# Kernel optimization log

Measured on AMD Instinct MI355X. Metric: run time of the kernel, lower is better.

## Reference

```python
import jax, jax.numpy as jnp
import numpy as np
import math

B, S, D, H = 4, 4096, 1024, 128

def setup_inputs() -> dict:
    key = jax.random.key(0)
    ks = jax.random.split(key, 4)
    scale = 1.0 / math.sqrt(D)
    return {
        "inputs": jax.random.normal(ks[0], (B, S, D), dtype=jnp.float32),
        "Wk": jax.random.normal(ks[1], (H, D), dtype=jnp.float32) * scale,
        "bk": jnp.zeros((H,), dtype=jnp.float32),
        "Wq": jax.random.normal(ks[2], (H, D), dtype=jnp.float32) * scale,
        "bq": jnp.zeros((H,), dtype=jnp.float32),
        "Wv": jax.random.normal(ks[3], (H, D), dtype=jnp.float32) * scale,
        "bv": jnp.zeros((H,), dtype=jnp.float32),
        "padding_mask": jnp.ones((B, S), dtype=jnp.int32),
    }

def reference(inputs, Wk, bk, Wq, bq, Wv, bv, padding_mask):
    # Linear projections: [B,S,D] x [H,D]^T -> [B,S,H]
    k = jnp.einsum('bsd,hd->bsh', inputs, Wk) + bk
    q = jnp.einsum('bsd,hd->bsh', inputs, Wq) + bq
    v = jnp.einsum('bsd,hd->bsh', inputs, Wv) + bv
    # Scaled dot-product scores: [B,S,S]
    scores = jnp.einsum('bqh,bkh->bqk', q, k) / jnp.sqrt(jnp.float32(k.shape[-1]))
    # Mask out padded key positions (mask==0 -> -1e9), broadcast over query dim
    scores = jnp.where(padding_mask[:, None, :] == 0, jnp.float32(-1e9), scores)
    weights = jax.nn.softmax(scores, axis=-1)
    # Dropout is identity in eval mode (reference runs inference / training=False)
    out = jnp.einsum('bqk,bkh->bqh', weights, v)
    return out
```

## Files before the change

kernel.cpp:

```cpp
#include <hip/hip_runtime.h>
#include <cmath>

#define B_ 4
#define S_ 4096
#define D_ 1024
#define H_ 128
#define M_ (B_*S_)
#define NQT 32

typedef _Float16 half8 __attribute__((ext_vector_type(8)));
typedef _Float16 half4 __attribute__((ext_vector_type(4)));
typedef float f32x4 __attribute__((ext_vector_type(4)));
typedef int i32x4 __attribute__((ext_vector_type(4)));

#define LOG2E 1.44269504088896340f

__device__ __forceinline__ void gload16(const void* g, void* l) {
    __builtin_amdgcn_global_load_lds(
        (const __attribute__((address_space(1))) unsigned int*)g,
        (__attribute__((address_space(3))) unsigned int*)l,
        16, 0, 0);
}

__global__ __launch_bounds__(256) void conv_w(
    const float* __restrict__ Wq, const float* __restrict__ Wk,
    const float* __restrict__ Wv, _Float16* __restrict__ wh)
{
    const int idx  = blockIdx.x * 256 + threadIdx.x;
    const int base = idx * 8;
    const int m    = base >> 17;
    const int off  = base & ((H_ * D_) - 1);
    const float* src = (m == 0 ? Wq : m == 1 ? Wk : Wv) + off;
    const float4 a = ((const float4*)src)[0];
    const float4 c = ((const float4*)src)[1];
    half8 h = { (_Float16)a.x, (_Float16)a.y, (_Float16)a.z, (_Float16)a.w,
                (_Float16)c.x, (_Float16)c.y, (_Float16)c.z, (_Float16)c.w };
    *(half8*)(wh + base) = h;
}

__global__ __launch_bounds__(256, 3) void proj_kernel(
    const float* __restrict__ x, const _Float16* __restrict__ wh,
    const float* __restrict__ bq, const float* __restrict__ bk,
    const float* __restrict__ bv,
    _Float16* __restrict__ qh, _Float16* __restrict__ kh,
    _Float16* __restrict__ vt)
{
    __shared__ _Float16 Xs[2][64][72];
    __shared__ _Float16 Ws2[2][128][64];

    const int t = threadIdx.x;
    const int yb = blockIdx.y;
    const float* __restrict__ bias = (yb == 0) ? bq : (yb == 1) ? bk : bv;
    const int m0 = blockIdx.x * 64;
    const int w = t >> 6, lane = t & 63;
    const int lg = lane >> 4, lr = lane & 15;

    f32x4 acc[8];
    #pragma unroll
    for (int i = 0; i < 8; ++i) acc[i] = f32x4{0.f, 0.f, 0.f, 0.f};

    const int xrow = t >> 2, xc = (t & 3) * 16;
    const float* xbase = x + (size_t)(m0 + xrow) * D_ + xc;

    int wbyte[4];
    #pragma unroll
    for (int i = 0; i < 4; ++i) {
        const int wrow = 32 * w + 8 * i + (lane >> 3);
        const int wblk = (lane & 7) ^ (lane >> 3);
        wbyte[i] = (wrow * D_ + wblk * 8) * 2;
    }
    const char* whb = (const char*)(wh + (size_t)yb * H_ * D_);

    float4 xfA[4], xfB[4];

#define WISSUE(KT, BUF)                                                       \
    {                                                                         \
        const char* wsrc = whb + (KT) * (64 * 2);                             \
        _Pragma("unroll")                                                     \
        for (int i = 0; i < 4; ++i)                                           \
            gload16(wsrc + wbyte[i], &Ws2[BUF][32 * w + 8 * i][0]);           \
    }
#define XISSUE(KT, XS)                                                        \
    {                                                                         \
        const float4* xs_ = (const float4*)(xbase + (KT) * 64);               \
        _Pragma("unroll") for (int i = 0; i < 4; ++i) XS[i] = xs_[i];         \
    }
#define XWRITE(XS, BUF)                                                       \
    {                                                                         \
        _Pragma("unroll") for (int i = 0; i < 4; ++i) {                       \
            half4 h = { (_Float16)XS[i].x, (_Float16)XS[i].y,                 \
                        (_Float16)XS[i].z, (_Float16)XS[i].w };               \
            *(half4*)&Xs[BUF][xrow][xc + 4 * i] = h;                          \
        }                                                                     \
    }
#define PMFMA(BUF)                                                            \
    {                                                                         \
        _Pragma("unroll") for (int kk = 0; kk < 2; ++kk) {                    \
            half8 a = *(const half8*)&Xs[BUF][w * 16 + lr][kk * 32 + 8 * lg]; \
            _Pragma("unroll") for (int ni = 0; ni < 8; ++ni) {                \
                half8 bfr = *(const half8*)&Ws2[BUF][ni * 16 + lr]            \
                                [((4 * kk + lg) ^ (lr & 7)) * 8];             \
                acc[ni] = __builtin_amdgcn_mfma_f32_16x16x32_f16(a, bfr, acc[ni], 0, 0, 0); \
            }                                                                 \
        }                                                                     \
    }

    WISSUE(0, 0)
    XISSUE(0, xfA)
    XISSUE(1, xfB)
    XWRITE(xfA, 0)
    __syncthreads();

    for (int kt = 0; kt < 16; kt += 2) {
        WISSUE(kt + 1, 1)
        if (kt + 2 < 16) XISSUE(kt + 2, xfA)
        PMFMA(0)
        XWRITE(xfB, 1)
        __syncthreads();
        if (kt + 2 < 16) WISSUE(kt + 2, 0)
        if (kt + 3 < 16) XISSUE(kt + 3, xfB)
        PMFMA(1)
        if (kt + 2 < 16) XWRITE(xfA, 0)
        __syncthreads();
    }
#undef WISSUE
#undef XISSUE
#undef XWRITE
#undef PMFMA

    const float qscale = 0.08838834764831845f * LOG2E;
    const int rowb = m0 + w * 16 + lg * 4;
    #pragma unroll
    for (int ni = 0; ni < 8; ++ni) {
        const int col = ni * 16 + lr;
        const float bval = bias[col];
        if (yb == 0) {
            #pragma unroll
            for (int r = 0; r < 4; ++r)
                qh[(size_t)(rowb + r) * H_ + col] = (_Float16)((acc[ni][r] + bval) * qscale);
        } else if (yb == 1) {
            #pragma unroll
            for (int r = 0; r < 4; ++r)
                kh[(size_t)(rowb + r) * H_ + col] = (_Float16)(acc[ni][r] + bval);
        } else {
            const int bb = rowb >> 12, s0 = rowb & (S_ - 1);
            half4 h;
            #pragma unroll
            for (int r = 0; r < 4; ++r) h[r] = (_Float16)(acc[ni][r] + bval);
            *(half4*)&vt[(size_t)bb * H_ * S_ + (size_t)col * S_ + s0] = h;
        }
    }
}

__device__ __forceinline__ void attn_tile2(
    const _Float16 (&Kb)[64][128], const _Float16 (&Vb)[128][64],
    const half8 (&qf)[2][4], f32x4 (&acc)[2][8], float (&m_)[2], float (&l_)[2],
    int muse, int lg, int lr, bool hi, int idx0, int idx1)
{
    const unsigned long long bz = __ballot(muse == 0);
    f32x4 sf[2][4];
    #pragma unroll
    for (int qs = 0; qs < 2; ++qs)
        #pragma unroll
        for (int i = 0; i < 4; ++i) sf[qs][i] = f32x4{0.f, 0.f, 0.f, 0.f};
    #pragma unroll
    for (int kk = 0; kk < 4; ++kk) {
        #pragma unroll
        for (int ni = 0; ni < 4; ++ni) {
            half8 kb = *(const half8*)&Kb[ni * 16 + lr][((4 * kk + lg) ^ (lr & 7)) * 8];
            #pragma unroll
            for (int qs = 0; qs < 2; ++qs)
                sf[qs][ni] = __builtin_amdgcn_mfma_f32_16x16x32_f16(kb, qf[qs][kk], sf[qs][ni], 0, 0, 0);
        }
    }

    i32x4 pbi[2][2];
    #pragma unroll
    for (int qs = 0; qs < 2; ++qs) {
        if (bz) {
            #pragma unroll
            for (int ni = 0; ni < 4; ++ni) {
                #pragma unroll
                for (int r = 0; r < 4; ++r)
                    if ((bz >> (16 * ni + 4 * lg + r)) & 1ull) sf[qs][ni][r] = -3e9f;
            }
        }
        float tmax = fmaxf(
            fmaxf(fmaxf(fmaxf(sf[qs][0][0], sf[qs][0][1]), fmaxf(sf[qs][0][2], sf[qs][0][3])),
                  fmaxf(fmaxf(sf[qs][1][0], sf[qs][1][1]), fmaxf(sf[qs][1][2], sf[qs][1][3]))),
            fmaxf(fmaxf(fmaxf(sf[qs][2][0], sf[qs][2][1]), fmaxf(sf[qs][2][2], sf[qs][2][3])),
                  fmaxf(fmaxf(sf[qs][3][0], sf[qs][3][1]), fmaxf(sf[qs][3][2], sf[qs][3][3]))));
        tmax = fmaxf(tmax, __shfl_xor(tmax, 16));
        tmax = fmaxf(tmax, __shfl_xor(tmax, 32));
        if (!__all(tmax <= m_[qs] + 8.f)) {
            const float mn  = fmaxf(m_[qs], tmax);
            const float scl = exp2f(m_[qs] - mn);
            m_[qs] = mn; l_[qs] *= scl;
            #pragma unroll
            for (int ni = 0; ni < 8; ++ni) acc[qs][ni] *= scl;
        }
        float rsum = 0.f;
        #pragma unroll
        for (int ni = 0; ni < 4; ++ni) {
            #pragma unroll
            for (int r = 0; r < 4; ++r) {
                const float p = exp2f(sf[qs][ni][r] - m_[qs]);
                sf[qs][ni][r] = p;
                rsum += p;
            }
        }
        rsum += __shfl_xor(rsum, 16);
        rsum += __shfl_xor(rsum, 32);
        l_[qs] += rsum;

        int pk[4][2];
        #pragma unroll
        for (int ni = 0; ni < 4; ++ni) {
            #pragma unroll
            for (int rp = 0; rp < 2; ++rp) {
                auto h2 = __builtin_amdgcn_cvt_pkrtz(sf[qs][ni][2 * rp], sf[qs][ni][2 * rp + 1]);
                pk[ni][rp] = __builtin_bit_cast(int, h2);
            }
        }
        #pragma unroll
        for (int kk = 0; kk < 2; ++kk) {
            #pragma unroll
            for (int dd = 0; dd < 4; ++dd) {
                const int sidx = (dd >> 1) ? idx1 : idx0;
                const int a  = __builtin_amdgcn_ds_bpermute(sidx, pk[2 * kk][dd & 1]);
                const int bb = __builtin_amdgcn_ds_bpermute(sidx, pk[2 * kk + 1][dd & 1]);
                pbi[qs][kk][dd] = hi ? bb : a;
            }
        }
    }
    #pragma unroll
    for (int kk = 0; kk < 2; ++kk) {
        #pragma unroll
        for (int ni = 0; ni < 8; ++ni) {
            half8 vb = *(const half8*)&Vb[ni * 16 + lr][((4 * kk + lg) ^ (lr & 7)) * 8];
            #pragma unroll
            for (int qs = 0; qs < 2; ++qs) {
                const half8 pb = __builtin_bit_cast(half8, pbi[qs][kk]);
                acc[qs][ni] = __builtin_amdgcn_mfma_f32_16x16x32_f16(vb, pb, acc[qs][ni], 0, 0, 0);
            }
        }
    }
}

__global__ __launch_bounds__(256, 2) void attn_kernel(
    const _Float16* __restrict__ qh, const _Float16* __restrict__ kh,
    const _Float16* __restrict__ vt, const int* __restrict__ mask,
    float* __restrict__ pout, float* __restrict__ pm, float* __restrict__ pl,
    const int nsplit)
{
    __shared__ _Float16 Ks[2][64][128];
    __shared__ _Float16 Vs[2][128][64];

    const int t = threadIdx.x;
    const int id = blockIdx.x;
    int qt, sp, b;
    const int ncombo = B_ * nsplit;
    if ((ncombo & 7) == 0) {
        const int per_xcd = ncombo >> 3;
        const int j = id >> 3;
        qt = j & (NQT - 1);
        const int combo = (id & 7) * per_xcd + (j >> 5);
        sp = combo % nsplit; b = combo / nsplit;
    } else {
        qt = id & (NQT - 1);
        const int rest = id >> 5;
        sp = rest % nsplit; b = rest / nsplit;
    }
    const int q0 = qt * 128;
    const int w = t >> 6, lane = t & 63;
    const int lg = lane >> 4, lr = lane & 15;
    const int kvlen  = S_ / nsplit;
    const int iters  = kvlen >> 6;
    const int kvbase = sp * kvlen;

    int kbyte[4], vbyte[4];
    #pragma unroll
    for (int i = 0; i < 4; ++i) {
        const int krow = 16 * w + 4 * i + (lane >> 4);
        const int kblk = (lane & 15) ^ (krow & 7);
        kbyte[i] = (krow * H_ + kblk * 8) * 2;
        const int vrow = 32 * w + 8 * i + (lane >> 3);
        const int vblk = (lane & 7) ^ (lane >> 3);
        vbyte[i] = (vrow * S_ + vblk * 8) * 2;
    }
    const char* kbase_b = (const char*)(kh + (size_t)(b * S_ + kvbase) * H_);
    const char* vbase_b = (const char*)(vt + (size_t)b * H_ * S_ + kvbase);
    const char* mbase_b = (const char*)(mask + b * S_ + kvbase + lane);

#define ISSUE_TILE(IT, NB)                                                    \
    {                                                                         \
        const char* kb_t = kbase_b + (size_t)(IT) * (64 * H_ * 2);            \
        const char* vb_t = vbase_b + (size_t)(IT) * (64 * 2);                 \
        _Pragma("unroll")                                                     \
        for (int i = 0; i < 4; ++i)                                           \
            gload16(kb_t + kbyte[i], &Ks[NB][16 * w + 4 * i][0]);             \
        _Pragma("unroll")                                                     \
        for (int i = 0; i < 4; ++i)                                           \
            gload16(vb_t + vbyte[i], &Vs[NB][32 * w + 8 * i][0]);             \
    }

    half8 qf[2][4];
    #pragma unroll
    for (int qs = 0; qs < 2; ++qs) {
        const _Float16* qp = qh + (size_t)(b * S_ + q0 + w * 32 + qs * 16 + lr) * H_ + 8 * lg;
        #pragma unroll
        for (int kk = 0; kk < 4; ++kk) qf[qs][kk] = *(const half8*)(qp + kk * 32);
    }

    float m_[2] = { -1e30f, -1e30f }, l_[2] = { 0.f, 0.f };
    f32x4 acc[2][8];
    #pragma unroll
    for (int qs = 0; qs < 2; ++qs)
        #pragma unroll
        for (int i = 0; i < 8; ++i) acc[qs][i] = f32x4{0.f, 0.f, 0.f, 0.f};

    const bool hi = (lg >= 2);
    const int idx0 = (16 * ((2 * lg + 0) & 3) + lr) * 4;
    const int idx1 = (16 * ((2 * lg + 1) & 3) + lr) * 4;

    ISSUE_TILE(0, 0)
    int mA = *(const int*)mbase_b;
    int mB = 0;
    __syncthreads();

    for (int it = 0; it < iters; it += 2) {
        if (it + 1 < iters) {
            ISSUE_TILE(it + 1, 1)
            mB = *(const int*)(mbase_b + (size_t)(it + 1) * 256);
        }
        attn_tile2(Ks[0], Vs[0], qf, acc, m_, l_, mA, lg, lr, hi, idx0, idx1);
        __syncthreads();
        if (it + 2 < iters) {
            ISSUE_TILE(it + 2, 0)
            mA = *(const int*)(mbase_b + (size_t)(it + 2) * 256);
        }
        if (it + 1 < iters)
            attn_tile2(Ks[1], Vs[1], qf, acc, m_, l_, mB, lg, lr, hi, idx0, idx1);
        __syncthreads();
    }
#undef ISSUE_TILE

    #pragma unroll
    for (int qs = 0; qs < 2; ++qs) {
        const int qrow = b * S_ + q0 + w * 32 + qs * 16 + lr;
        float* op = pout + (size_t)(sp * M_ + qrow) * H_ + 4 * lg;
        #pragma unroll
        for (int ni = 0; ni < 8; ++ni)
            *(f32x4*)(op + 16 * ni) = acc[qs][ni];
        if (lg == 0) {
            pm[sp * M_ + qrow] = m_[qs];
            pl[sp * M_ + qrow] = l_[qs];
        }
    }
}

__global__ __launch_bounds__(256) void combine_kernel(
    const float* __restrict__ pout, const float* __restrict__ pm,
    const float* __restrict__ pl, float* __restrict__ out, const int nsplit)
{
    const int idx = blockIdx.x * 256 + threadIdx.x;
    const int row = idx >> 7;
    const int h   = idx & (H_ - 1);
    float M = -1e30f;
    for (int sp = 0; sp < nsplit; ++sp) M = fmaxf(M, pm[sp * M_ + row]);
    float Z = 0.f, o = 0.f;
    for (int sp = 0; sp < nsplit; ++sp) {
        const float wgt = exp2f(pm[sp * M_ + row] - M);
        Z += wgt * pl[sp * M_ + row];
        o += wgt * pout[(size_t)(sp * M_ + row) * H_ + h];
    }
    out[idx] = o / Z;
}

extern "C" void kernel_launch(void* const* d_in, const int* in_sizes, int n_in,
                              void* d_out, int out_size, void* d_ws, size_t ws_size,
                              hipStream_t stream)
{
    (void)in_sizes; (void)n_in; (void)out_size;
    const float* x  = (const float*)d_in[0];
    const float* Wk = (const float*)d_in[1];
    const float* bk = (const float*)d_in[2];
    const float* Wq = (const float*)d_in[3];
    const float* bq = (const float*)d_in[4];
    const float* Wv = (const float*)d_in[5];
    const float* bv = (const float*)d_in[6];
    const int* mask = (const int*)d_in[7];

    char* ws = (char*)d_ws;
    const size_t qkvBytes = (size_t)M_ * H_ * sizeof(_Float16);
    _Float16* qh = (_Float16*)ws;
    _Float16* kh = (_Float16*)(ws + qkvBytes);
    _Float16* vt = (_Float16*)(ws + 2 * qkvBytes);
    _Float16* wh = (_Float16*)(ws + 3 * qkvBytes);
    const size_t whBytes = (size_t)3 * H_ * D_ * sizeof(_Float16);
    char* rest = ws + 3 * qkvBytes + whBytes;

    int nsplit = 4;
    const size_t perSplit = (size_t)M_ * H_ * 4 + 2 * (size_t)M_ * 4;
    while (nsplit > 1 &&
           3 * qkvBytes + whBytes + (size_t)nsplit * perSplit > ws_size) nsplit >>= 1;

    float* pout = (float*)rest;
    float* pm   = (float*)(rest + (size_t)nsplit * M_ * H_ * 4);
    float* pl   = pm + (size_t)nsplit * M_;

    conv_w<<<dim3(3 * H_ * D_ / (256 * 8)), 256, 0, stream>>>(Wq, Wk, Wv, wh);
    proj_kernel<<<dim3(M_ / 64, 3), 256, 0, stream>>>(x, wh, bq, bk, bv, qh, kh, vt);
    attn_kernel<<<dim3(NQT * B_ * nsplit), 256, 0, stream>>>(qh, kh, vt, mask, pout, pm, pl, nsplit);
    combine_kernel<<<dim3(M_ * H_ / 256), 256, 0, stream>>>(pout, pm, pl, (float*)d_out, nsplit);
}
```

Measured before the change: 112.5 us.

## Switch attention inner loop to 32x32x16 MFMA with shuffle-based P relayout

Rewrites the per-tile attention computation to use 32x32x16 f16 MFMA instructions instead of 16x16x32, with each wave handling 32 query rows as a single block. The softmax row reductions need only one cross-lane shuffle, and the P-to-operand relayout uses xor-32 shuffles instead of ds_bpermute. The aim is fewer MFMA issues and less cross-lane traffic per tile. In exchange the 16-wide accumulators raise register pressure, and the output stores become scattered float2 writes.

Result: faster. 109.9 us (-2.3%).

```diff
diff --git a/kernel.cpp b/kernel.cpp
--- a/kernel.cpp
+++ b/kernel.cpp
@@ -11,6 +11,7 @@
 typedef _Float16 half8 __attribute__((ext_vector_type(8)));
 typedef _Float16 half4 __attribute__((ext_vector_type(4)));
 typedef float f32x4 __attribute__((ext_vector_type(4)));
+typedef float f32x16 __attribute__((ext_vector_type(16)));
 typedef int i32x4 __attribute__((ext_vector_type(4)));
 
 #define LOG2E 1.44269504088896340f
@@ -152,97 +153,95 @@
     }
 }
 
-__device__ __forceinline__ void attn_tile2(
+__device__ __forceinline__ void attn_tile32(
     const _Float16 (&Kb)[64][128], const _Float16 (&Vb)[128][64],
-    const half8 (&qf)[2][4], f32x4 (&acc)[2][8], float (&m_)[2], float (&l_)[2],
-    int muse, int lg, int lr, bool hi, int idx0, int idx1)
+    const half8 (&qf)[8], f32x16 (&acc2)[4], float& m_, float& l_,
+    int muse, int lane)
 {
     const unsigned long long bz = __ballot(muse == 0);
-    f32x4 sf[2][4];
-    #pragma unroll
-    for (int qs = 0; qs < 2; ++qs)
-        #pragma unroll
-        for (int i = 0; i < 4; ++i) sf[qs][i] = f32x4{0.f, 0.f, 0.f, 0.f};
-    #pragma unroll
-    for (int kk = 0; kk < 4; ++kk) {
-        #pragma unroll
-        for (int ni = 0; ni < 4; ++ni) {
-            half8 kb = *(const half8*)&Kb[ni * 16 + lr][((4 * kk + lg) ^ (lr & 7)) * 8];
+    const int l31 = lane & 31, l7 = lane & 7, hi = lane >> 5;
+
+    f32x16 sf[2];
+    #pragma unroll
+    for (int nb = 0; nb < 2; ++nb)
+        #pragma unroll
+        for (int r = 0; r < 16; ++r) sf[nb][r] = 0.f;
+    #pragma unroll
+    for (int kt = 0; kt < 8; ++kt) {
+        #pragma unroll
+        for (int nb = 0; nb < 2; ++nb) {
+            half8 kb = *(const half8*)&Kb[nb * 32 + l31][((2 * kt + hi) ^ l7) * 8];
+            sf[nb] = __builtin_amdgcn_mfma_f32_32x32x16_f16(kb, qf[kt], sf[nb], 0, 0, 0);
+        }
+    }
+    if (bz) {
+        #pragma unroll
+        for (int nb = 0; nb < 2; ++nb)
             #pragma unroll
-            for (int qs = 0; qs < 2; ++qs)
-                sf[qs][ni] = __builtin_amdgcn_mfma_f32_16x16x32_f16(kb, qf[qs][kk], sf[qs][ni], 0, 0, 0);
-        }
-    }
-
-    i32x4 pbi[2][2];
-    #pragma unroll
-    for (int qs = 0; qs < 2; ++qs) {
-        if (bz) {
-            #pragma unroll
-            for (int ni = 0; ni < 4; ++ni) {
-                #pragma unroll
-                for (int r = 0; r < 4; ++r)
-                    if ((bz >> (16 * ni + 4 * lg + r)) & 1ull) sf[qs][ni][r] = -3e9f;
+            for (int r = 0; r < 16; ++r) {
+                const int kv = nb * 32 + (r & 3) + 8 * (r >> 2) + 4 * hi;
+                if ((bz >> kv) & 1ull) sf[nb][r] = -3e9f;
             }
-        }
-        float tmax = fmaxf(
-            fmaxf(fmaxf(fmaxf(sf[qs][0][0], sf[qs][0][1]), fmaxf(sf[qs][0][2], sf[qs][0][3])),
-                  fmaxf(fmaxf(sf[qs][1][0], sf[qs][1][1]), fmaxf(sf[qs][1][2], sf[qs][1][3]))),
-            fmaxf(fmaxf(fmaxf(sf[qs][2][0], sf[qs][2][1]), fmaxf(sf[qs][2][2], sf[qs][2][3])),
-                  fmaxf(fmaxf(sf[qs][3][0], sf[qs][3][1]), fmaxf(sf[qs][3][2], sf[qs][3][3]))));
-        tmax = fmaxf(tmax, __shfl_xor(tmax, 16));
-        tmax = fmaxf(tmax, __shfl_xor(tmax, 32));
-        if (!__all(tmax <= m_[qs] + 8.f)) {
-            const float mn  = fmaxf(m_[qs], tmax);
-            const float scl = exp2f(m_[qs] - mn);
-            m_[qs] = mn; l_[qs] *= scl;
-            #pragma unroll
-            for (int ni = 0; ni < 8; ++ni) acc[qs][ni] *= scl;
-        }
-        float rsum = 0.f;
-        #pragma unroll
-        for (int ni = 0; ni < 4; ++ni) {
-            #pragma unroll
-            for (int r = 0; r < 4; ++r) {
-                const float p = exp2f(sf[qs][ni][r] - m_[qs]);
-                sf[qs][ni][r] = p;
-                rsum += p;
-            }
-        }
-        rsum += __shfl_xor(rsum, 16);
-        rsum += __shfl_xor(rsum, 32);
-        l_[qs] += rsum;
-
-        int pk[4][2];
-        #pragma unroll
-        for (int ni = 0; ni < 4; ++ni) {
-            #pragma unroll
-            for (int rp = 0; rp < 2; ++rp) {
-                auto h2 = __builtin_amdgcn_cvt_pkrtz(sf[qs][ni][2 * rp], sf[qs][ni][2 * rp + 1]);
-                pk[ni][rp] = __builtin_bit_cast(int, h2);
-            }
-        }
-        #pragma unroll
-        for (int kk = 0; kk < 2; ++kk) {
-            #pragma unroll
-            for (int dd = 0; dd < 4; ++dd) {
-                const int sidx = (dd >> 1) ? idx1 : idx0;
-                const int a  = __builtin_amdgcn_ds_bpermute(sidx, pk[2 * kk][dd & 1]);
-                const int bb = __builtin_amdgcn_ds_bpermute(sidx, pk[2 * kk + 1][dd & 1]);
-                pbi[qs][kk][dd] = hi ? bb : a;
-            }
-        }
-    }
-    #pragma unroll
-    for (int kk = 0; kk < 2; ++kk) {
-        #pragma unroll
-        for (int ni = 0; ni < 8; ++ni) {
-            half8 vb = *(const half8*)&Vb[ni * 16 + lr][((4 * kk + lg) ^ (lr & 7)) * 8];
-            #pragma unroll
-            for (int qs = 0; qs < 2; ++qs) {
-                const half8 pb = __builtin_bit_cast(half8, pbi[qs][kk]);
-                acc[qs][ni] = __builtin_amdgcn_mfma_f32_16x16x32_f16(vb, pb, acc[qs][ni], 0, 0, 0);
-            }
+    }
+    float tmax = sf[0][0];
+    #pragma unroll
+    for (int nb = 0; nb < 2; ++nb)
+        #pragma unroll
+        for (int r = 0; r < 16; ++r) tmax = fmaxf(tmax, sf[nb][r]);
+    tmax = fmaxf(tmax, __shfl_xor(tmax, 32));
+    if (!__all(tmax <= m_ + 8.f)) {
+        const float mn  = fmaxf(m_, tmax);
+        const float scl = exp2f(m_ - mn);
+        m_ = mn; l_ *= scl;
+        #pragma unroll
+        for (int hb = 0; hb < 4; ++hb) acc2[hb] *= scl;
+    }
+    float rsum = 0.f;
+    #pragma unroll
+    for (int nb = 0; nb < 2; ++nb)
+        #pragma unroll
+        for (int r = 0; r < 16; ++r) {
+            const float p = exp2f(sf[nb][r] - m_);
+            sf[nb][r] = p;
+            rsum += p;
+        }
+    rsum += __shfl_xor(rsum, 32);
+    l_ += rsum;
+
+    int pkw[2][8];
+    #pragma unroll
+    for (int nb = 0; nb < 2; ++nb)
+        #pragma unroll
+        for (int i = 0; i < 8; ++i) {
+            auto h2 = __builtin_amdgcn_cvt_pkrtz(sf[nb][2 * i], sf[nb][2 * i + 1]);
+            pkw[nb][i] = __builtin_bit_cast(int, h2);
+        }
+    #pragma unroll
+    for (int nb = 0; nb < 2; ++nb)
+        #pragma unroll
+        for (int hf = 0; hf < 2; ++hf) {
+            const int i0 = hf * 4;
+            const int sA = hi ? pkw[nb][i0 + 0] : pkw[nb][i0 + 2];
+            const int sB = hi ? pkw[nb][i0 + 1] : pkw[nb][i0 + 3];
+            const int rA = __shfl_xor(sA, 32);
+            const int rB = __shfl_xor(sB, 32);
+            const int n0 = hi ? rA : pkw[nb][i0 + 0];
+            const int n1 = hi ? rB : pkw[nb][i0 + 1];
+            const int n2 = hi ? pkw[nb][i0 + 2] : rA;
+            const int n3 = hi ? pkw[nb][i0 + 3] : rB;
+            pkw[nb][i0 + 0] = n0; pkw[nb][i0 + 1] = n1;
+            pkw[nb][i0 + 2] = n2; pkw[nb][i0 + 3] = n3;
+        }
+    #pragma unroll
+    for (int s = 0; s < 4; ++s) {
+        const int nb = s >> 1, hf = s & 1;
+        const half8 pb = __builtin_bit_cast(half8,
+            i32x4{ pkw[nb][hf * 4 + 0], pkw[nb][hf * 4 + 1],
+                   pkw[nb][hf * 4 + 2], pkw[nb][hf * 4 + 3] });
+        #pragma unroll
+        for (int hb = 0; hb < 4; ++hb) {
+            half8 vb = *(const half8*)&Vb[hb * 32 + l31][((2 * s + hi) ^ l7) * 8];
+            acc2[hb] = __builtin_amdgcn_mfma_f32_32x32x16_f16(vb, pb, acc2[hb], 0, 0, 0);
         }
     }
 }
@@ -273,7 +272,7 @@
     }
     const int q0 = qt * 128;
     const int w = t >> 6, lane = t & 63;
-    const int lg = lane >> 4, lr = lane & 15;
+    const int l31 = lane & 31, hi = lane >> 5;
     const int kvlen  = S_ / nsplit;
     const int iters  = kvlen >> 6;
     const int kvbase = sp * kvlen;
@@ -304,24 +303,19 @@
             gload16(vb_t + vbyte[i], &Vs[NB][32 * w + 8 * i][0]);             \
     }
 
-    half8 qf[2][4];
-    #pragma unroll
-    for (int qs = 0; qs < 2; ++qs) {
-        const _Float16* qp = qh + (size_t)(b * S_ + q0 + w * 32 + qs * 16 + lr) * H_ + 8 * lg;
-        #pragma unroll
-        for (int kk = 0; kk < 4; ++kk) qf[qs][kk] = *(const half8*)(qp + kk * 32);
-    }
-
-    float m_[2] = { -1e30f, -1e30f }, l_[2] = { 0.f, 0.f };
-    f32x4 acc[2][8];
-    #pragma unroll
-    for (int qs = 0; qs < 2; ++qs)
-        #pragma unroll
-        for (int i = 0; i < 8; ++i) acc[qs][i] = f32x4{0.f, 0.f, 0.f, 0.f};
-
-    const bool hi = (lg >= 2);
-    const int idx0 = (16 * ((2 * lg + 0) & 3) + lr) * 4;
-    const int idx1 = (16 * ((2 * lg + 1) & 3) + lr) * 4;
+    half8 qf[8];
+    {
+        const _Float16* qp = qh + (size_t)(b * S_ + q0 + 32 * w + l31) * H_ + 8 * hi;
+        #pragma unroll
+        for (int kt = 0; kt < 8; ++kt) qf[kt] = *(const half8*)(qp + 16 * kt);
+    }
+
+    float m_ = -1e30f, l_ = 0.f;
+    f32x16 acc2[4];
+    #pragma unroll
+    for (int hb = 0; hb < 4; ++hb)
+        #pragma unroll
+        for (int r = 0; r < 16; ++r) acc2[hb][r] = 0.f;
 
     ISSUE_TILE(0, 0)
     int mA = *(const int*)mbase_b;
@@ -333,29 +327,31 @@
             ISSUE_TILE(it + 1, 1)
             mB = *(const int*)(mbase_b + (size_t)(it + 1) * 256);
         }
-        attn_tile2(Ks[0], Vs[0], qf, acc, m_, l_, mA, lg, lr, hi, idx0, idx1);
+        attn_tile32(Ks[0], Vs[0], qf, acc2, m_, l_, mA, lane);
         __syncthreads();
         if (it + 2 < iters) {
             ISSUE_TILE(it + 2, 0)
             mA = *(const int*)(mbase_b + (size_t)(it + 2) * 256);
         }
         if (it + 1 < iters)
-            attn_tile2(Ks[1], Vs[1], qf, acc, m_, l_, mB, lg, lr, hi, idx0, idx1);
+            attn_tile32(Ks[1], Vs[1], qf, acc2, m_, l_, mB, lane);
         __syncthreads();
     }
 #undef ISSUE_TILE
 
-    #pragma unroll
-    for (int qs = 0; qs < 2; ++qs) {
-        const int qrow = b * S_ + q0 + w * 32 + qs * 16 + lr;
-        float* op = pout + (size_t)(sp * M_ + qrow) * H_ + 4 * lg;
-        #pragma unroll
-        for (int ni = 0; ni < 8; ++ni)
-            *(f32x4*)(op + 16 * ni) = acc[qs][ni];
-        if (lg == 0) {
-            pm[sp * M_ + qrow] = m_[qs];
-            pl[sp * M_ + qrow] = l_[qs];
-        }
+    const int qrow = b * S_ + q0 + 32 * w + l31;
+    float* op = pout + (size_t)(sp * M_ + qrow) * H_;
+    #pragma unroll
+    for (int hb = 0; hb < 4; ++hb)
+        #pragma unroll
+        for (int i = 0; i < 8; ++i) {
+            const int h = hb * 32 + 2 * (i & 1) + 8 * (i >> 1) + 4 * hi;
+            float2 v2 = make_float2(acc2[hb][2 * i], acc2[hb][2 * i + 1]);
+            *(float2*)(op + h) = v2;
+        }
+    if (hi == 0) {
+        pm[sp * M_ + qrow] = m_;
+        pl[sp * M_ + qrow] = l_;
     }
 }
 
```
